# Performance work log

Measured on AMD Instinct MI355X. Metric: run time of the kernel, lower is better.

The kernel has to match this reference:

```python
import jax, jax.numpy as jnp
import numpy as np

B, H, W, DIM = 16, 64, 64, 256
EXPAND = 2
D_INNER = DIM * EXPAND      # 512
HID = D_INNER // 2          # 256 per GRU direction


def setup_inputs() -> dict:
    ks = jax.random.split(jax.random.key(0), 10)
    g = lambda i, shape, s=0.05: jax.random.normal(ks[i], shape, dtype=jnp.float32) * s
    return {
        "x": jax.random.normal(ks[0], (B, H, W, DIM), dtype=jnp.float32),
        "ln_gamma": jnp.ones((DIM,), jnp.float32),
        "ln_beta": jnp.zeros((DIM,), jnp.float32),
        "mlp_w1": g(1, (32, 4), 0.3),
        "mlp_b1": jnp.zeros((32,), jnp.float32),
        "mlp_w2": g(2, (4, 32), 0.3),
        "mlp_b2": jnp.zeros((4,), jnp.float32),
        "in_w": g(3, (D_INNER, DIM)),
        "in_b": jnp.zeros((D_INNER,), jnp.float32),
        "gru_wih_f": g(4, (3 * HID, D_INNER)),
        "gru_whh_f": g(5, (3 * HID, HID)),
        "gru_bih_f": jnp.zeros((3 * HID,), jnp.float32),
        "gru_bhh_f": jnp.zeros((3 * HID,), jnp.float32),
        "gru_wih_b": g(6, (3 * HID, D_INNER)),
        "gru_whh_b": g(7, (3 * HID, HID)),
        "gru_bih_b": jnp.zeros((3 * HID,), jnp.float32),
        "gru_bhh_b": jnp.zeros((3 * HID,), jnp.float32),
        "out_w": g(8, (DIM, D_INNER)),
        "out_b": jnp.zeros((DIM,), jnp.float32),
    }


def _resize_linear_axis(x, out_size, axis):
    """torch F.interpolate(mode='bilinear', align_corners=False) along one axis
    (the other axis has scale 1 -> identity, so 1-D resize is exact)."""
    in_size = x.shape[axis]
    scale = in_size / out_size
    src = (jnp.arange(out_size, dtype=jnp.float32) + 0.5) * scale - 0.5
    src = jnp.clip(src, 0.0, in_size - 1)
    i0 = jnp.floor(src).astype(jnp.int32)
    i1 = jnp.minimum(i0 + 1, in_size - 1)
    w = (src - i0.astype(jnp.float32))
    x0 = jnp.take(x, i0, axis=axis)
    x1 = jnp.take(x, i1, axis=axis)
    shape = [1] * x.ndim
    shape[axis] = out_size
    w = w.reshape(shape)
    return x0 * (1.0 - w) + x1 * w


def _avgpool3_mean(g):
    """F.avg_pool2d(g, 3, stride=1, padding=1) (count_include_pad=True), then
    spatial mean -> [B, 1]."""
    s = jax.lax.reduce_window(g, 0.0, jax.lax.add, (1, 1, 3, 3), (1, 1, 1, 1),
                              [(0, 0), (0, 0), (1, 1), (1, 1)])
    return (s / 9.0).mean(axis=(2, 3))


def _gru_dir(xp, whh, bhh, reverse):
    """One GRU direction. xp: [B, L, 3h] precomputed input-side gates."""
    hid = whh.shape[1]
    h0 = jnp.zeros((xp.shape[0], hid), xp.dtype)

    def step(h, xt):
        gh = h @ whh.T + bhh
        xr, xz, xn = jnp.split(xt, 3, axis=-1)
        hr, hz, hn = jnp.split(gh, 3, axis=-1)
        r = jax.nn.sigmoid(xr + hr)
        z = jax.nn.sigmoid(xz + hz)
        n = jnp.tanh(xn + r * hn)
        h_new = (1.0 - z) * n + z * h
        return h_new, h_new

    _, ys = jax.lax.scan(step, h0, jnp.swapaxes(xp, 0, 1), reverse=reverse)
    return jnp.swapaxes(ys, 0, 1)  # [B, L, h], ys[t] aligned with input t


def _forward(x, ln_gamma, ln_beta, mlp_w1, mlp_b1, mlp_w2, mlp_b2,
             in_w, in_b, gru_wih_f, gru_whh_f, gru_bih_f, gru_bhh_f,
             gru_wih_b, gru_whh_b, gru_bih_b, gru_bhh_b, out_w, out_b):
    Bx, Hx, Wx, C = x.shape
    # LayerNorm over channels
    mu = x.mean(-1, keepdims=True)
    var = ((x - mu) ** 2).mean(-1, keepdims=True)
    xn = (x - mu) / jnp.sqrt(var + 1e-5) * ln_gamma + ln_beta

    # --- GradientDirectionSelector ---
    gray = xn.mean(-1)[:, None]                                   # [B,1,H,W]
    gp = jnp.pad(gray, ((0, 0), (0, 0), (1, 1), (1, 1)), mode="reflect")
    grad_h = jnp.abs(gp[:, :, :, 2:] - gp[:, :, :, :-2])          # [B,1,H+2,W]
    grad_v = jnp.abs(gp[:, :, 2:, :] - gp[:, :, :-2, :])          # [B,1,H,W+2]
    grad_h = _resize_linear_axis(grad_h, Hx, axis=2)              # [B,1,H,W]
    grad_v = _resize_linear_axis(grad_v, Wx, axis=3)              # [B,1,H,W]
    grad_d = (grad_h + grad_v) * 0.5
    grad_a = jnp.abs(grad_h - grad_v)
    scores = jnp.concatenate(
        [_avgpool3_mean(g) for g in (grad_h, grad_v, grad_d, grad_a)], axis=1)  # [B,4]
    h1 = jax.nn.relu(scores @ mlp_w1.T + mlp_b1)
    logits = h1 @ mlp_w2.T + mlp_b2
    probs = jax.nn.softmax(logits, axis=-1)
    idx = jnp.argmax(probs, axis=-1)  # topk=1 indices, [B]

    # --- direction-routed scan (dir 1 -> vertical transpose; 0/2/3 -> row-major) ---
    seq_h = xn.reshape(Bx, Hx * Wx, C)
    seq_v = jnp.swapaxes(xn, 1, 2).reshape(Bx, Hx * Wx, C)
    seq = jnp.where((idx == 1)[:, None, None], seq_v, seq_h)      # [B,L,C]

    # --- FastSequenceBlock: in_proj -> biGRU -> out_proj ---
    z = seq @ in_w.T + in_b                                       # [B,L,d_inner]
    yf = _gru_dir(z @ gru_wih_f.T + gru_bih_f, gru_whh_f, gru_bhh_f, False)
    yb = _gru_dir(z @ gru_wih_b.T + gru_bih_b, gru_whh_b, gru_bhh_b, True)
    y = jnp.concatenate([yf, yb], axis=-1) @ out_w.T + out_b      # [B,L,C]

    # unscan (row-major reshape, as in the original) + residual
    return x + y.reshape(Bx, Hx, Wx, C)


def reference(x, ln_gamma, ln_beta, mlp_w1, mlp_b1, mlp_w2, mlp_b2,
              in_w, in_b, gru_wih_f, gru_whh_f, gru_bih_f, gru_bhh_f,
              gru_wih_b, gru_whh_b, gru_bih_b, gru_bhh_b, out_w, out_b):
    return _forward(x, ln_gamma, ln_beta, mlp_w1, mlp_b1, mlp_w2, mlp_b2,
                    in_w, in_b, gru_wih_f, gru_whh_f, gru_bih_f, gru_bhh_f,
                    gru_wih_b, gru_whh_b, gru_bih_b, gru_bhh_b, out_w, out_b)
```

## Files before the change

### kernel.cpp

```cpp
#include <hip/hip_runtime.h>


#define L_   4096
#define CH   32
#define NCH  128

typedef __attribute__((ext_vector_type(8))) _Float16 half8;
typedef __attribute__((ext_vector_type(4))) float f32x4;

__device__ __forceinline__ unsigned short f2h(float f) {
  _Float16 h = (_Float16)f;
  return __builtin_bit_cast(unsigned short, h);
}
__device__ __forceinline__ float h2f(unsigned short u) {
  return (float)__builtin_bit_cast(_Float16, u);
}
__device__ __forceinline__ float sigm(float x) {
  return __builtin_amdgcn_rcpf(1.f + __expf(-x));
}
__device__ __forceinline__ float tanhf_(float x) {
  return 1.f - 2.f * __builtin_amdgcn_rcpf(1.f + __expf(2.f * x));
}

__global__ __launch_bounds__(256) void k_f2h(const float* __restrict__ in,
                                             unsigned short* __restrict__ out,
                                             int n) {
  int i = blockIdx.x * 256 + threadIdx.x;
  if (i < n) out[i] = f2h(in[i]);
}

__global__ __launch_bounds__(256) void k_whhP(const float* __restrict__ whh_f,
                                              const float* __restrict__ whh_b,
                                              unsigned short* __restrict__ whhP) {
  const int x = blockIdx.x;
  const int dir = x >= 768;
  const int p = dir ? (x - 768) : x;
  const int w = p / 96;
  const int r = p - w * 96;
  const int j = r >> 4;
  const int l = r & 15;
  const int g = j >> 1;
  const int u = w * 32 + (j & 1) * 16 + l;
  const float* src = (dir ? whh_b : whh_f) + (long)(g * 256 + u) * 256;
  whhP[(long)x * 256 + threadIdx.x] = f2h(src[threadIdx.x]);
}

__global__ __launch_bounds__(256) void k_wcomb(const float* __restrict__ wih_f,
                                               const float* __restrict__ wih_b,
                                               const float* __restrict__ in_w,
                                               unsigned short* __restrict__ wcomb) {
  const int n = blockIdx.x;
  const float* wrow = (n < 768) ? (wih_f + (long)n * 512)
                                : (wih_b + (long)(n - 768) * 512);
  const int k = threadIdx.x;
  float acc = 0.f;
  for (int j = 0; j < 512; ++j) acc += wrow[j] * in_w[j * 256 + k];
  wcomb[(long)n * 256 + k] = f2h(acc);
}

__global__ __launch_bounds__(256) void k_bcomb(const float* __restrict__ wih_f,
                                               const float* __restrict__ wih_b,
                                               const float* __restrict__ in_b,
                                               const float* __restrict__ bih_f,
                                               const float* __restrict__ bih_b,
                                               float* __restrict__ bcomb) {
  int n = blockIdx.x * 256 + threadIdx.x;
  if (n >= 1536) return;
  const float* wrow = (n < 768) ? (wih_f + (long)n * 512)
                                : (wih_b + (long)(n - 768) * 512);
  float acc = (n < 768) ? bih_f[n] : bih_b[n - 768];
  for (int j = 0; j < 512; ++j) acc += wrow[j] * in_b[j];
  bcomb[n] = acc;
}

__global__ __launch_bounds__(256) void k_ln(const float* __restrict__ x,
                                            const float* __restrict__ gamma,
                                            const float* __restrict__ beta,
                                            unsigned short* __restrict__ xn,
                                            float* __restrict__ gray) {
  const int lane = threadIdx.x & 63;
  const long pix = (long)blockIdx.x * 4 + (threadIdx.x >> 6);
  const float4 v = *(const float4*)(x + pix * 256 + lane * 4);
  float s = v.x + v.y + v.z + v.w;
  float s2 = v.x * v.x + v.y * v.y + v.z * v.z + v.w * v.w;
#pragma unroll
  for (int off = 32; off > 0; off >>= 1) {
    s += __shfl_xor(s, off, 64);
    s2 += __shfl_xor(s2, off, 64);
  }
  const float mu = s * (1.f / 256.f);
  const float var = fmaxf(s2 * (1.f / 256.f) - mu * mu, 0.f);
  const float rstd = rsqrtf(var + 1e-5f);
  const float4 gm = *(const float4*)(gamma + lane * 4);
  const float4 bt = *(const float4*)(beta + lane * 4);
  float o0 = (v.x - mu) * rstd * gm.x + bt.x;
  float o1 = (v.y - mu) * rstd * gm.y + bt.y;
  float o2 = (v.z - mu) * rstd * gm.z + bt.z;
  float o3 = (v.w - mu) * rstd * gm.w + bt.w;
  ushort4 o;
  o.x = f2h(o0); o.y = f2h(o1); o.z = f2h(o2); o.w = f2h(o3);
  *(ushort4*)(xn + pix * 256 + lane * 4) = o;
  float gs = o0 + o1 + o2 + o3;
#pragma unroll
  for (int off = 32; off > 0; off >>= 1) gs += __shfl_xor(gs, off, 64);
  if (lane == 0) gray[pix] = gs * (1.f / 256.f);
}

__device__ __forceinline__ int refl64(int m) {
  return m < 0 ? -m : (m > 63 ? 126 - m : m);
}

__global__ __launch_bounds__(256) void k_sel(const float* __restrict__ gray,
                                             const float* __restrict__ w1,
                                             const float* __restrict__ b1,
                                             const float* __restrict__ w2,
                                             const float* __restrict__ b2,
                                             int* __restrict__ flag) {
  __shared__ float g[64][65];
  __shared__ float part[4][4];
  const int b = blockIdx.x;
  const int tid = threadIdx.x;
  for (int r = 0; r < 16; ++r) {
    int p = tid + 256 * r;
    g[p >> 6][p & 63] = gray[(long)b * 4096 + p];
  }
  __syncthreads();
  const float S = 66.f / 64.f;
  float sh = 0.f, sv = 0.f, sd = 0.f, sa = 0.f;
  for (int rr = 0; rr < 16; ++rr) {
    int p = tid + 256 * rr;
    int h = p >> 6, w = p & 63;
    float srci = (h + 0.5f) * S - 0.5f;
    int i0 = (int)srci;
    float ai = srci - (float)i0;
    int i1 = i0 + 1; if (i1 > 65) i1 = 65;
    int r0 = refl64(i0 - 1), r1 = refl64(i1 - 1);
    int wl = w ? (w - 1) : 1;
    int wr2 = (w == 63) ? 62 : (w + 1);
    float GH0 = fabsf(g[r0][wr2] - g[r0][wl]);
    float GH1 = fabsf(g[r1][wr2] - g[r1][wl]);
    float ghr = GH0 + ai * (GH1 - GH0);
    float srcj = (w + 0.5f) * S - 0.5f;
    int j0 = (int)srcj;
    float aj = srcj - (float)j0;
    int j1 = j0 + 1; if (j1 > 65) j1 = 65;
    int c0 = refl64(j0 - 1), c1 = refl64(j1 - 1);
    int hu = h ? (h - 1) : 1;
    int hd = (h == 63) ? 62 : (h + 1);
    float GV0 = fabsf(g[hd][c0] - g[hu][c0]);
    float GV1 = fabsf(g[hd][c1] - g[hu][c1]);
    float gvr = GV0 + aj * (GV1 - GV0);
    float wt = ((h == 0 || h == 63) ? 2.f : 3.f) *
               ((w == 0 || w == 63) ? 2.f : 3.f);
    sh += wt * ghr;
    sv += wt * gvr;
    sd += wt * 0.5f * (ghr + gvr);
    sa += wt * fabsf(ghr - gvr);
  }
#pragma unroll
  for (int off = 32; off > 0; off >>= 1) {
    sh += __shfl_xor(sh, off, 64);
    sv += __shfl_xor(sv, off, 64);
    sd += __shfl_xor(sd, off, 64);
    sa += __shfl_xor(sa, off, 64);
  }
  if ((tid & 63) == 0) {
    part[tid >> 6][0] = sh; part[tid >> 6][1] = sv;
    part[tid >> 6][2] = sd; part[tid >> 6][3] = sa;
  }
  __syncthreads();
  if (tid == 0) {
    float sc[4];
    for (int k = 0; k < 4; ++k)
      sc[k] = (part[0][k] + part[1][k] + part[2][k] + part[3][k]) * (1.f / 36864.f);
    float logits[4];
    for (int k = 0; k < 4; ++k) logits[k] = b2[k];
    for (int j = 0; j < 32; ++j) {
      float hj = b1[j];
      for (int i = 0; i < 4; ++i) hj += sc[i] * w1[j * 4 + i];
      hj = fmaxf(hj, 0.f);
      for (int k = 0; k < 4; ++k) logits[k] += hj * w2[k * 32 + j];
    }
    int idx = 0;
    float best = logits[0];
    for (int k = 1; k < 4; ++k)
      if (logits[k] > best) { best = logits[k]; idx = k; }
    flag[b] = (idx == 1) ? 1 : 0;
  }
}

__global__ __launch_bounds__(256) void k_gemm(const unsigned short* __restrict__ A,
                                              const unsigned short* __restrict__ Bw,
                                              const float* __restrict__ bias,
                                              const float* __restrict__ resid,
                                              float* __restrict__ out,
                                              int K, int N) {
  __shared__ unsigned short Al[128][40];
  __shared__ unsigned short Bl[128][40];
  const int tid = threadIdx.x;
  const long m0 = (long)blockIdx.x * 128;
  const int n0 = blockIdx.y * 128;
  const int rA = tid >> 2;
  const int cp = (tid & 3) * 8;

  const unsigned short* a0p = A + (m0 + rA) * K + cp;
  const unsigned short* a1p = A + (m0 + rA + 64) * K + cp;
  const unsigned short* b0p = Bw + (long)(n0 + rA) * K + cp;
  const unsigned short* b1p = Bw + (long)(n0 + rA + 64) * K + cp;

  const int wv = tid >> 6, lane = tid & 63;
  const int wm = (wv >> 1) * 64, wn = (wv & 1) * 64;
  const int fr = lane & 15, fq = lane >> 4;

  const f32x4 zero4 = {0.f, 0.f, 0.f, 0.f};
  f32x4 acc[4][4];
#pragma unroll
  for (int i = 0; i < 4; ++i)
#pragma unroll
    for (int j = 0; j < 4; ++j) acc[i][j] = zero4;

  for (int k0 = 0; k0 < K; k0 += 32) {
    half8 va0 = *(const half8*)(a0p + k0);
    half8 va1 = *(const half8*)(a1p + k0);
    half8 vb0 = *(const half8*)(b0p + k0);
    half8 vb1 = *(const half8*)(b1p + k0);
    __syncthreads();
    *(half8*)&Al[rA][cp] = va0;
    *(half8*)&Al[rA + 64][cp] = va1;
    *(half8*)&Bl[rA][cp] = vb0;
    *(half8*)&Bl[rA + 64][cp] = vb1;
    __syncthreads();
    half8 af[4], bf[4];
#pragma unroll
    for (int i = 0; i < 4; ++i) af[i] = *(const half8*)&Al[wm + i * 16 + fr][fq * 8];
#pragma unroll
    for (int j = 0; j < 4; ++j) bf[j] = *(const half8*)&Bl[wn + j * 16 + fr][fq * 8];
#pragma unroll
    for (int i = 0; i < 4; ++i)
#pragma unroll
      for (int j = 0; j < 4; ++j)
        acc[i][j] = __builtin_amdgcn_mfma_f32_16x16x32_f16(af[i], bf[j], acc[i][j], 0, 0, 0);
  }

#pragma unroll
  for (int j = 0; j < 4; ++j) {
    const int col = n0 + wn + j * 16 + fr;
    const float bv = bias[col];
#pragma unroll
    for (int i = 0; i < 4; ++i) {
      const long mbase = m0 + wm + i * 16 + fq * 4;
#pragma unroll
      for (int r = 0; r < 4; ++r) {
        const long m = mbase + r;
        out[m * N + col] = acc[i][j][r] + bv + resid[m * N + col];
      }
    }
  }
}

__global__ __launch_bounds__(512, 2) void k_scan(
    const unsigned short* __restrict__ xn,
    const unsigned short* __restrict__ wcomb,
    const float* __restrict__ bcomb,
    const unsigned short* __restrict__ whhP,
    const float* __restrict__ bhhf,
    const float* __restrict__ bhhb,
    const int* __restrict__ flag,
    unsigned short* __restrict__ ycat) {
  const int dir = blockIdx.x & 1;
  const int b = blockIdx.x >> 1;
  const unsigned short* whh = whhP + (long)dir * (768 * 256);
  const float* bhh = dir ? bhhb : bhhf;
  const unsigned short* wcd = wcomb + (long)dir * (768 * 256);
  const float* bcd = bcomb + dir * 768;
  const int tid = threadIdx.x;
  const int wv = tid >> 6;
  const int lane = tid & 63;
  const int fr = lane & 15;
  const int fq = lane >> 4;
  const int fb = flag[b];

  half8 wf[6][8];
#pragma unroll
  for (int j = 0; j < 6; ++j) {
    const unsigned short* wrow =
        whh + (long)((wv * 6 + j) * 16 + fr) * 256 + fq * 8;
#pragma unroll
    for (int s = 0; s < 8; ++s) wf[j][s] = *(const half8*)(wrow + s * 32);
  }

  __shared__ unsigned short xplds[CH][768];
  __shared__ unsigned short ylds[CH][256];
  __shared__ unsigned short hbuf[2][256];

  const int u0 = wv * 32 + fr;
  float Br0 = 0.f, Br1 = 0.f, Bz0 = 0.f, Bz1 = 0.f;
  float Bnh0 = 0.f, Bnh1 = 0.f, Bcn0 = 0.f, Bcn1 = 0.f;
  float h0 = 0.f, h1 = 0.f;
  if (lane < 16) {
    Br0 = bhh[u0] + bcd[u0];
    Br1 = bhh[u0 + 16] + bcd[u0 + 16];
    Bz0 = bhh[256 + u0] + bcd[256 + u0];
    Bz1 = bhh[256 + u0 + 16] + bcd[256 + u0 + 16];
    Bnh0 = bhh[512 + u0];
    Bnh1 = bhh[512 + u0 + 16];
    Bcn0 = bcd[512 + u0];
    Bcn1 = bcd[512 + u0 + 16];
  }
  if (tid < 256) hbuf[0][tid] = 0;
  __syncthreads();

  const long xnb = (long)b * 4096;
  unsigned short* yb = ycat + (long)b * (L_ * 512) + dir * 256;

  const f32x4 zero4 = {0.f, 0.f, 0.f, 0.f};
  const half8 zero8h = {0, 0, 0, 0, 0, 0, 0, 0};
  int pb = 0;

  for (int c = 0; c < NCH; ++c) {
    const int cc = dir ? (NCH - 1 - c) : c;
    const int t0 = cc * CH;

    if (c > 0) {
      const int pt0 = (dir ? (NCH - c) : (c - 1)) * CH;
#pragma unroll
      for (int k = 0; k < 2; ++k) {
        const int idx = tid * 2 + k;
        const int ts = idx >> 5;
        const int cl = (idx & 31) * 8;
        half8 v = *(const half8*)&ylds[ts][cl];
        *(half8*)(yb + (long)(pt0 + ts) * 512 + cl) = v;
      }
    }

    const unsigned short* arow0;
    const unsigned short* arow1;
    {
      int t = t0 + fr;
      int p = fb ? (((t & 63) << 6) | (t >> 6)) : t;
      arow0 = xn + (xnb + p) * 256 + fq * 8;
      t = t0 + 16 + fr;
      p = fb ? (((t & 63) << 6) | (t >> 6)) : t;
      arow1 = xn + (xnb + p) * 256 + fq * 8;
    }
#pragma unroll
    for (int hf = 0; hf < 2; ++hf) {
      f32x4 acc0[3], acc1[3];
#pragma unroll
      for (int j = 0; j < 3; ++j) { acc0[j] = zero4; acc1[j] = zero4; }
#pragma unroll
      for (int s = 0; s < 8; ++s) {
        half8 a0 = *(const half8*)(arow0 + s * 32);
        half8 a1 = *(const half8*)(arow1 + s * 32);
#pragma unroll
        for (int j = 0; j < 3; ++j) {
          const int n = wv * 96 + hf * 48 + j * 16 + fr;
          half8 bfr = *(const half8*)(wcd + (long)n * 256 + s * 32 + fq * 8);
          acc0[j] = __builtin_amdgcn_mfma_f32_16x16x32_f16(a0, bfr, acc0[j], 0, 0, 0);
          acc1[j] = __builtin_amdgcn_mfma_f32_16x16x32_f16(a1, bfr, acc1[j], 0, 0, 0);
        }
      }
#pragma unroll
      for (int j = 0; j < 3; ++j) {
        const int n = wv * 96 + hf * 48 + j * 16 + fr;
#pragma unroll
        for (int r = 0; r < 4; ++r) {
          xplds[fq * 4 + r][n] = f2h(acc0[j][r]);
          xplds[16 + fq * 4 + r][n] = f2h(acc1[j][r]);
        }
      }
    }
    __syncthreads();

    for (int lt = 0; lt < CH; ++lt) {
      const int ts = dir ? (CH - 1 - lt) : lt;
      float xr0 = 0.f, xr1 = 0.f, xz0 = 0.f, xz1 = 0.f, xn0 = 0.f, xn1 = 0.f;
      if (lane < 16) {
        xr0 = h2f(xplds[ts][u0]);
        xr1 = h2f(xplds[ts][u0 + 16]);
        xz0 = h2f(xplds[ts][256 + u0]);
        xz1 = h2f(xplds[ts][256 + u0 + 16]);
        xn0 = h2f(xplds[ts][512 + u0]);
        xn1 = h2f(xplds[ts][512 + u0 + 16]);
      }
      f32x4 acc[6];
#pragma unroll
      for (int s = 0; s < 8; ++s) {
        half8 a = zero8h;
        if (fr == 0) a = *(const half8*)&hbuf[pb][s * 32 + fq * 8];
#pragma unroll
        for (int j = 0; j < 6; ++j) {
          f32x4 cin = (s == 0) ? zero4 : acc[j];
          acc[j] = __builtin_amdgcn_mfma_f32_16x16x32_f16(a, wf[j][s], cin, 0, 0, 0);
        }
      }
      if (lane < 16) {
        float r0 = sigm(xr0 + acc[0][0] + Br0);
        float r1 = sigm(xr1 + acc[1][0] + Br1);
        float z0 = sigm(xz0 + acc[2][0] + Bz0);
        float z1 = sigm(xz1 + acc[3][0] + Bz1);
        float n0 = tanhf_(xn0 + Bcn0 + r0 * (acc[4][0] + Bnh0));
        float n1 = tanhf_(xn1 + Bcn1 + r1 * (acc[5][0] + Bnh1));
        h0 = n0 + z0 * (h0 - n0);
        h1 = n1 + z1 * (h1 - n1);
        unsigned short hb0 = f2h(h0);
        unsigned short hb1 = f2h(h1);
        hbuf[pb ^ 1][u0] = hb0;
        hbuf[pb ^ 1][u0 + 16] = hb1;
        ylds[ts][u0] = hb0;
        ylds[ts][u0 + 16] = hb1;
      }
      pb ^= 1;
      __syncthreads();
    }
  }
  {
    const int pt0 = (dir ? 0 : (NCH - 1)) * CH;
#pragma unroll
    for (int k = 0; k < 2; ++k) {
      const int idx = tid * 2 + k;
      const int ts = idx >> 5;
      const int cl = (idx & 31) * 8;
      half8 v = *(const half8*)&ylds[ts][cl];
      *(half8*)(yb + (long)(pt0 + ts) * 512 + cl) = v;
    }
  }
}

extern "C" void kernel_launch(void* const* d_in, const int* in_sizes, int n_in,
                              void* d_out, int out_size, void* d_ws, size_t ws_size,
                              hipStream_t stream) {
  (void)in_sizes; (void)n_in; (void)out_size; (void)ws_size;
  const float* x     = (const float*)d_in[0];
  const float* lng   = (const float*)d_in[1];
  const float* lnb   = (const float*)d_in[2];
  const float* w1    = (const float*)d_in[3];
  const float* b1    = (const float*)d_in[4];
  const float* w2    = (const float*)d_in[5];
  const float* b2    = (const float*)d_in[6];
  const float* in_w  = (const float*)d_in[7];
  const float* in_b  = (const float*)d_in[8];
  const float* wih_f = (const float*)d_in[9];
  const float* whh_f = (const float*)d_in[10];
  const float* bih_f = (const float*)d_in[11];
  const float* bhh_f = (const float*)d_in[12];
  const float* wih_b = (const float*)d_in[13];
  const float* whh_b = (const float*)d_in[14];
  const float* bih_b = (const float*)d_in[15];
  const float* bhh_b = (const float*)d_in[16];
  const float* out_w = (const float*)d_in[17];
  const float* out_b = (const float*)d_in[18];

  char* ws = (char*)d_ws;
  unsigned short* xn     = (unsigned short*)(ws + 0);
  float*          gray   = (float*)(ws + 33554432);
  int*            flag   = (int*)(ws + 33816576);
  unsigned short* whhP   = (unsigned short*)(ws + 33816832);
  unsigned short* outw16 = (unsigned short*)(ws + 34603264);
  unsigned short* wcomb  = (unsigned short*)(ws + 34865408);
  float*          bcomb  = (float*)(ws + 35651840);
  unsigned short* ycat   = (unsigned short*)(ws + 35658240);

  k_whhP<<<1536, 256, 0, stream>>>(whh_f, whh_b, whhP);
  k_f2h<<<512, 256, 0, stream>>>(out_w, outw16, 131072);
  k_wcomb<<<1536, 256, 0, stream>>>(wih_f, wih_b, in_w, wcomb);
  k_bcomb<<<6, 256, 0, stream>>>(wih_f, wih_b, in_b, bih_f, bih_b, bcomb);
  k_ln<<<16384, 256, 0, stream>>>(x, lng, lnb, xn, gray);
  k_sel<<<16, 256, 0, stream>>>(gray, w1, b1, w2, b2, flag);
  k_scan<<<32, 512, 0, stream>>>(xn, wcomb, bcomb, whhP,
                                 bhh_f, bhh_b, flag, ycat);
  dim3 gout(512, 2);
  k_gemm<<<gout, 256, 0, stream>>>(ycat, outw16, out_b, x, (float*)d_out, 512, 256);
}
```

Baseline: 7.382 ms.

## Halve GRU scan block to 4 waves, each owning 64 hidden units

The recurrent scan kernel now runs with 256 threads (4 waves) instead of 512. Each wave holds 12 register-resident Whh fragments covering 64 hidden units, and the weight permutation kernel is changed to match. Fewer waves should cut the per-timestep __syncthreads cost on the serial critical path. The input biases (plus the r/z parts of bhh) are folded into the projection result before it is written to LDS, and the branchy zero-fill of the A operand is replaced by a read from a zeroed padding slot. The cost is much higher register pressure and fewer waves sharing the input-projection and gate work.

```diff
diff --git a/kernel.cpp b/kernel.cpp
--- a/kernel.cpp
+++ b/kernel.cpp
@@ -35,12 +35,12 @@
   const int x = blockIdx.x;
   const int dir = x >= 768;
   const int p = dir ? (x - 768) : x;
-  const int w = p / 96;
-  const int r = p - w * 96;
-  const int j = r >> 4;
-  const int l = r & 15;
-  const int g = j >> 1;
-  const int u = w * 32 + (j & 1) * 16 + l;
+  const int wv = p / 192;
+  const int r2 = p - wv * 192;
+  const int j = r2 >> 4;
+  const int l = r2 & 15;
+  const int g = j >> 2;
+  const int u = wv * 64 + (j & 3) * 16 + l;
   const float* src = (dir ? whh_b : whh_f) + (long)(g * 256 + u) * 256;
   whhP[(long)x * 256 + threadIdx.x] = f2h(src[threadIdx.x]);
 }
@@ -63,14 +63,18 @@
                                                const float* __restrict__ in_b,
                                                const float* __restrict__ bih_f,
                                                const float* __restrict__ bih_b,
-                                               float* __restrict__ bcomb) {
+                                               const float* __restrict__ bhh_f,
+                                               const float* __restrict__ bhh_b,
+                                               float* __restrict__ badj) {
   int n = blockIdx.x * 256 + threadIdx.x;
   if (n >= 1536) return;
-  const float* wrow = (n < 768) ? (wih_f + (long)n * 512)
-                                : (wih_b + (long)(n - 768) * 512);
-  float acc = (n < 768) ? bih_f[n] : bih_b[n - 768];
+  const int dir = n >= 768;
+  const int g = dir ? (n - 768) : n;
+  const float* wrow = (dir ? wih_b : wih_f) + (long)g * 512;
+  float acc = (dir ? bih_b : bih_f)[g];
   for (int j = 0; j < 512; ++j) acc += wrow[j] * in_b[j];
-  bcomb[n] = acc;
+  if (g < 512) acc += (dir ? bhh_b : bhh_f)[g];
+  badj[n] = acc;
 }
 
 __global__ __launch_bounds__(256) void k_ln(const float* __restrict__ x,
@@ -258,10 +262,10 @@
   }
 }
 
-__global__ __launch_bounds__(512, 2) void k_scan(
+__global__ __launch_bounds__(256, 1) void k_scan(
     const unsigned short* __restrict__ xn,
     const unsigned short* __restrict__ wcomb,
-    const float* __restrict__ bcomb,
+    const float* __restrict__ badj,
     const unsigned short* __restrict__ whhP,
     const float* __restrict__ bhhf,
     const float* __restrict__ bhhb,
@@ -272,7 +276,7 @@
   const unsigned short* whh = whhP + (long)dir * (768 * 256);
   const float* bhh = dir ? bhhb : bhhf;
   const unsigned short* wcd = wcomb + (long)dir * (768 * 256);
-  const float* bcd = bcomb + dir * 768;
+  const float* bcd = badj + dir * 768;
   const int tid = threadIdx.x;
   const int wv = tid >> 6;
   const int lane = tid & 63;
@@ -280,41 +284,41 @@
   const int fq = lane >> 4;
   const int fb = flag[b];
 
-  half8 wf[6][8];
-#pragma unroll
-  for (int j = 0; j < 6; ++j) {
+  half8 wf[12][8];
+#pragma unroll
+  for (int j = 0; j < 12; ++j) {
     const unsigned short* wrow =
-        whh + (long)((wv * 6 + j) * 16 + fr) * 256 + fq * 8;
+        whh + (long)((wv * 12 + j) * 16 + fr) * 256 + fq * 8;
 #pragma unroll
     for (int s = 0; s < 8; ++s) wf[j][s] = *(const half8*)(wrow + s * 32);
   }
+#pragma unroll
+  for (int j = 0; j < 12; ++j)
+#pragma unroll
+    for (int s = 0; s < 8; ++s) asm volatile("" : "+v"(wf[j][s]));
 
   __shared__ unsigned short xplds[CH][768];
   __shared__ unsigned short ylds[CH][256];
-  __shared__ unsigned short hbuf[2][256];
-
-  const int u0 = wv * 32 + fr;
-  float Br0 = 0.f, Br1 = 0.f, Bz0 = 0.f, Bz1 = 0.f;
-  float Bnh0 = 0.f, Bnh1 = 0.f, Bcn0 = 0.f, Bcn1 = 0.f;
-  float h0 = 0.f, h1 = 0.f;
+  __shared__ unsigned short hbuf[2][272];
+
+  float Bnh[4], h[4];
+#pragma unroll
+  for (int q = 0; q < 4; ++q) { Bnh[q] = 0.f; h[q] = 0.f; }
   if (lane < 16) {
-    Br0 = bhh[u0] + bcd[u0];
-    Br1 = bhh[u0 + 16] + bcd[u0 + 16];
-    Bz0 = bhh[256 + u0] + bcd[256 + u0];
-    Bz1 = bhh[256 + u0 + 16] + bcd[256 + u0 + 16];
-    Bnh0 = bhh[512 + u0];
-    Bnh1 = bhh[512 + u0 + 16];
-    Bcn0 = bcd[512 + u0];
-    Bcn1 = bcd[512 + u0 + 16];
-  }
-  if (tid < 256) hbuf[0][tid] = 0;
+#pragma unroll
+    for (int q = 0; q < 4; ++q) Bnh[q] = bhh[512 + wv * 64 + q * 16 + fr];
+  }
+  hbuf[0][tid] = 0;
+  if (tid < 16) {
+    hbuf[0][256 + tid] = 0;
+    hbuf[1][256 + tid] = 0;
+  }
   __syncthreads();
 
   const long xnb = (long)b * 4096;
   unsigned short* yb = ycat + (long)b * (L_ * 512) + dir * 256;
 
   const f32x4 zero4 = {0.f, 0.f, 0.f, 0.f};
-  const half8 zero8h = {0, 0, 0, 0, 0, 0, 0, 0};
   int pb = 0;
 
   for (int c = 0; c < NCH; ++c) {
@@ -324,8 +328,8 @@
     if (c > 0) {
       const int pt0 = (dir ? (NCH - c) : (c - 1)) * CH;
 #pragma unroll
-      for (int k = 0; k < 2; ++k) {
-        const int idx = tid * 2 + k;
+      for (int k = 0; k < 4; ++k) {
+        const int idx = tid + 256 * k;
         const int ts = idx >> 5;
         const int cl = (idx & 31) * 8;
         half8 v = *(const half8*)&ylds[ts][cl];
@@ -344,7 +348,7 @@
       arow1 = xn + (xnb + p) * 256 + fq * 8;
     }
 #pragma unroll
-    for (int hf = 0; hf < 2; ++hf) {
+    for (int hf = 0; hf < 4; ++hf) {
       f32x4 acc0[3], acc1[3];
 #pragma unroll
       for (int j = 0; j < 3; ++j) { acc0[j] = zero4; acc1[j] = zero4; }
@@ -354,7 +358,7 @@
         half8 a1 = *(const half8*)(arow1 + s * 32);
 #pragma unroll
         for (int j = 0; j < 3; ++j) {
-          const int n = wv * 96 + hf * 48 + j * 16 + fr;
+          const int n = wv * 192 + hf * 48 + j * 16 + fr;
           half8 bfr = *(const half8*)(wcd + (long)n * 256 + s * 32 + fq * 8);
           acc0[j] = __builtin_amdgcn_mfma_f32_16x16x32_f16(a0, bfr, acc0[j], 0, 0, 0);
           acc1[j] = __builtin_amdgcn_mfma_f32_16x16x32_f16(a1, bfr, acc1[j], 0, 0, 0);
@@ -362,11 +366,12 @@
       }
 #pragma unroll
       for (int j = 0; j < 3; ++j) {
-        const int n = wv * 96 + hf * 48 + j * 16 + fr;
+        const int n = wv * 192 + hf * 48 + j * 16 + fr;
+        const float bv = bcd[n];
 #pragma unroll
         for (int r = 0; r < 4; ++r) {
-          xplds[fq * 4 + r][n] = f2h(acc0[j][r]);
-          xplds[16 + fq * 4 + r][n] = f2h(acc1[j][r]);
+          xplds[fq * 4 + r][n] = f2h(acc0[j][r] + bv);
+          xplds[16 + fq * 4 + r][n] = f2h(acc1[j][r] + bv);
         }
       }
     }
@@ -374,41 +379,41 @@
 
     for (int lt = 0; lt < CH; ++lt) {
       const int ts = dir ? (CH - 1 - lt) : lt;
-      float xr0 = 0.f, xr1 = 0.f, xz0 = 0.f, xz1 = 0.f, xn0 = 0.f, xn1 = 0.f;
+      float xr[4], xz[4], xnv[4];
+#pragma unroll
+      for (int q = 0; q < 4; ++q) { xr[q] = 0.f; xz[q] = 0.f; xnv[q] = 0.f; }
       if (lane < 16) {
-        xr0 = h2f(xplds[ts][u0]);
-        xr1 = h2f(xplds[ts][u0 + 16]);
-        xz0 = h2f(xplds[ts][256 + u0]);
-        xz1 = h2f(xplds[ts][256 + u0 + 16]);
-        xn0 = h2f(xplds[ts][512 + u0]);
-        xn1 = h2f(xplds[ts][512 + u0 + 16]);
-      }
-      f32x4 acc[6];
+#pragma unroll
+        for (int q = 0; q < 4; ++q) {
+          const int u = wv * 64 + q * 16 + fr;
+          xr[q] = h2f(xplds[ts][u]);
+          xz[q] = h2f(xplds[ts][256 + u]);
+          xnv[q] = h2f(xplds[ts][512 + u]);
+        }
+      }
+      f32x4 acc[12];
+#pragma unroll
+      for (int j = 0; j < 12; ++j) acc[j] = zero4;
 #pragma unroll
       for (int s = 0; s < 8; ++s) {
-        half8 a = zero8h;
-        if (fr == 0) a = *(const half8*)&hbuf[pb][s * 32 + fq * 8];
-#pragma unroll
-        for (int j = 0; j < 6; ++j) {
-          f32x4 cin = (s == 0) ? zero4 : acc[j];
-          acc[j] = __builtin_amdgcn_mfma_f32_16x16x32_f16(a, wf[j][s], cin, 0, 0, 0);
+        const half8 a =
+            *(const half8*)&hbuf[pb][(fr == 0) ? (s * 32 + fq * 8) : 256];
+#pragma unroll
+        for (int j = 0; j < 12; ++j)
+          acc[j] = __builtin_amdgcn_mfma_f32_16x16x32_f16(a, wf[j][s], acc[j], 0, 0, 0);
+      }
+      if (lane < 16) {
+#pragma unroll
+        for (int q = 0; q < 4; ++q) {
+          const int u = wv * 64 + q * 16 + fr;
+          float r = sigm(xr[q] + acc[q][0]);
+          float z = sigm(xz[q] + acc[4 + q][0]);
+          float n = tanhf_(xnv[q] + r * (acc[8 + q][0] + Bnh[q]));
+          h[q] = n + z * (h[q] - n);
+          unsigned short hb = f2h(h[q]);
+          hbuf[pb ^ 1][u] = hb;
+          ylds[ts][u] = hb;
         }
-      }
-      if (lane < 16) {
-        float r0 = sigm(xr0 + acc[0][0] + Br0);
-        float r1 = sigm(xr1 + acc[1][0] + Br1);
-        float z0 = sigm(xz0 + acc[2][0] + Bz0);
-        float z1 = sigm(xz1 + acc[3][0] + Bz1);
-        float n0 = tanhf_(xn0 + Bcn0 + r0 * (acc[4][0] + Bnh0));
-        float n1 = tanhf_(xn1 + Bcn1 + r1 * (acc[5][0] + Bnh1));
-        h0 = n0 + z0 * (h0 - n0);
-        h1 = n1 + z1 * (h1 - n1);
-        unsigned short hb0 = f2h(h0);
-        unsigned short hb1 = f2h(h1);
-        hbuf[pb ^ 1][u0] = hb0;
-        hbuf[pb ^ 1][u0 + 16] = hb1;
-        ylds[ts][u0] = hb0;
-        ylds[ts][u0 + 16] = hb1;
       }
       pb ^= 1;
       __syncthreads();
@@ -417,8 +422,8 @@
   {
     const int pt0 = (dir ? 0 : (NCH - 1)) * CH;
 #pragma unroll
-    for (int k = 0; k < 2; ++k) {
-      const int idx = tid * 2 + k;
+    for (int k = 0; k < 4; ++k) {
+      const int idx = tid + 256 * k;
       const int ts = idx >> 5;
       const int cl = (idx & 31) * 8;
       half8 v = *(const half8*)&ylds[ts][cl];
@@ -458,16 +463,17 @@
   unsigned short* whhP   = (unsigned short*)(ws + 33816832);
   unsigned short* outw16 = (unsigned short*)(ws + 34603264);
   unsigned short* wcomb  = (unsigned short*)(ws + 34865408);
-  float*          bcomb  = (float*)(ws + 35651840);
+  float*          badj   = (float*)(ws + 35651840);
   unsigned short* ycat   = (unsigned short*)(ws + 35658240);
 
   k_whhP<<<1536, 256, 0, stream>>>(whh_f, whh_b, whhP);
   k_f2h<<<512, 256, 0, stream>>>(out_w, outw16, 131072);
   k_wcomb<<<1536, 256, 0, stream>>>(wih_f, wih_b, in_w, wcomb);
-  k_bcomb<<<6, 256, 0, stream>>>(wih_f, wih_b, in_b, bih_f, bih_b, bcomb);
+  k_bcomb<<<6, 256, 0, stream>>>(wih_f, wih_b, in_b, bih_f, bih_b,
+                                 bhh_f, bhh_b, badj);
   k_ln<<<16384, 256, 0, stream>>>(x, lng, lnb, xn, gray);
   k_sel<<<16, 256, 0, stream>>>(gray, w1, b1, w2, b2, flag);
-  k_scan<<<32, 512, 0, stream>>>(xn, wcomb, bcomb, whhP,
+  k_scan<<<32, 256, 0, stream>>>(xn, wcomb, badj, whhP,
                                  bhh_f, bhh_b, flag, ycat);
   dim3 gout(512, 2);
   k_gemm<<<gout, 256, 0, stream>>>(ycat, outw16, out_b, x, (float*)d_out, 512, 256);
```

Result: slower. 9.060 ms (+22.7%).
